# Kernel tuning notes

Hardware: AMD Instinct MI355X
Metric: run time of the kernel (lower is better)

## Reference

```python
import jax, jax.numpy as jnp
import numpy as np

T, H, I, E, TOPK = 4096, 2048, 4096, 8, 2


def setup_inputs() -> dict:
    key = jax.random.key(0)
    k0, k1, k2, k3, k4, k5 = jax.random.split(key, 6)
    return {
        "hidden_states": jax.random.normal(k0, (T, H), dtype=jnp.float32),
        "expert_affinities": jax.random.uniform(k1, (T, E), dtype=jnp.float32),
        "expert_index": jax.random.randint(k2, (T, TOPK), 0, E),
        "w_gate": jax.random.normal(k3, (E, H, I), dtype=jnp.float32) / np.float32(np.sqrt(H)),
        "w_up": jax.random.normal(k4, (E, H, I), dtype=jnp.float32) / np.float32(np.sqrt(H)),
        "w_down": jax.random.normal(k5, (E, I, H), dtype=jnp.float32) / np.float32(np.sqrt(I)),
    }


def reference(hidden_states, expert_affinities, expert_index, w_gate, w_up, w_down):
    num_experts = w_gate.shape[0]
    # top_k-hot mask (T, E); duplicate expert picks accumulate, matching torch loop
    expert_mask = jnp.sum(jax.nn.one_hot(expert_index, num_experts, dtype=jnp.float32), axis=1)
    # mask affinities to chosen experts, then L1-normalize (F.normalize p=1, eps=1e-12)
    aff = jnp.where(expert_mask == 0, 0.0, expert_affinities)
    aff = aff / jnp.maximum(jnp.sum(jnp.abs(aff), axis=1, keepdims=True), 1e-12)
    # all-experts GLU MLP: every expert processes all tokens
    g = jnp.einsum('th,ehi->eti', hidden_states, w_gate)   # (E, T, I)
    u = jnp.einsum('th,ehi->eti', hidden_states, w_up)     # (E, T, I)
    h = jax.nn.silu(g) * u                                  # (E, T, I)
    out_e = jnp.einsum('eti,eih->eth', h, w_down)           # (E, T, H)
    # affinity-weighted combine across experts
    return jnp.einsum('eth,te->th', out_e, aff)             # (T, H)
```

## Files before the change

### kernel.cpp

```cpp
#include <hip/hip_runtime.h>
#include <hip/hip_bf16.h>


constexpr int kT   = 4096;
constexpr int kH   = 2048;
constexpr int kI   = 4096;
constexpr int kE   = 8;
constexpr int kCap = 4096;
constexpr int kRowsCap = 10240;

typedef __attribute__((ext_vector_type(8))) short bf16x8;
typedef __attribute__((ext_vector_type(4))) float f32x4;

constexpr size_t HSB_OFF  = 0;
constexpr size_t HBUF_OFF = 16777216;
constexpr size_t RA_OFF   = HBUF_OFF + (size_t)kRowsCap * kI * 2;
constexpr size_t RB_OFF   = RA_OFF + (size_t)kE * kH * kI * 2;
constexpr size_t CNT_OFF  = RB_OFF + (size_t)kE * kH * kI * 2;
constexpr size_t OFF_OFF  = CNT_OFF + 256;
constexpr size_t LTOK_OFF = OFF_OFF + 256;
constexpr size_t LW_OFF   = LTOK_OFF + (size_t)kE * kCap * 4;
constexpr size_t POS_OFF  = LW_OFF + (size_t)kE * kCap * 4;
constexpr size_t WROW_OFF = POS_OFF + (size_t)kT * 2 * 4;

__device__ __forceinline__ unsigned short f2bf(float x) {
  unsigned int u = __float_as_uint(x);
  u += 0x7FFFu + ((u >> 16) & 1u);
  return (unsigned short)(u >> 16);
}
__device__ __forceinline__ unsigned pk2(float a, float b) {
  return (unsigned)f2bf(a) | ((unsigned)f2bf(b) << 16);
}
__device__ __forceinline__ float silu_f(float x) { return x / (1.f + __expf(-x)); }

__device__ __forceinline__ void async_copy16(void* lds, const void* g) {
  __builtin_amdgcn_global_load_lds(
      (const __attribute__((address_space(1))) void*)g,
      (__attribute__((address_space(3))) void*)lds, 16, 0, 0);
}

#define MFMA_BF16 __builtin_amdgcn_mfma_f32_16x16x32_bf16

__global__ void cvt_hs_kernel(const float* __restrict__ in, unsigned short* __restrict__ out) {
  size_t i = ((size_t)blockIdx.x * 256 + threadIdx.x) * 8;
  float4 a = *(const float4*)(in + i);
  float4 b = *(const float4*)(in + i + 4);
  uint4 v;
  v.x = pk2(a.x, a.y); v.y = pk2(a.z, a.w);
  v.z = pk2(b.x, b.y); v.w = pk2(b.z, b.w);
  *(uint4*)(out + i) = v;
}

__global__ __launch_bounds__(256)
void tcvt_kernel(const float* __restrict__ src, unsigned short* __restrict__ dst,
                 int K, int N) {
  __shared__ __attribute__((aligned(16))) unsigned short s[64][72];
  const size_t mat = (size_t)K * N;
  const float* S = src + (size_t)blockIdx.z * mat;
  unsigned short* D = dst + (size_t)blockIdx.z * mat;
  const int k0 = blockIdx.y * 64, n0 = blockIdx.x * 64;
  const int t  = threadIdx.x;
  const int n4 = (t & 15) * 4;
  const int k4 = (t >> 4) * 4;
  const float* p0 = S + (size_t)(k0 + k4) * N + n0 + n4;
  float4 r0 = *(const float4*)(p0);
  float4 r1 = *(const float4*)(p0 + N);
  float4 r2 = *(const float4*)(p0 + 2 * (size_t)N);
  float4 r3 = *(const float4*)(p0 + 3 * (size_t)N);
  uint2 v;
  v.x = pk2(r0.x, r1.x); v.y = pk2(r2.x, r3.x); *(uint2*)(&s[n4 + 0][k4]) = v;
  v.x = pk2(r0.y, r1.y); v.y = pk2(r2.y, r3.y); *(uint2*)(&s[n4 + 1][k4]) = v;
  v.x = pk2(r0.z, r1.z); v.y = pk2(r2.z, r3.z); *(uint2*)(&s[n4 + 2][k4]) = v;
  v.x = pk2(r0.w, r1.w); v.y = pk2(r2.w, r3.w); *(uint2*)(&s[n4 + 3][k4]) = v;
  __syncthreads();
  const int nn = t >> 3;
  const int kc = (t & 7) * 8;
#pragma unroll
  for (int i = 0; i < 2; ++i) {
    const int n = nn + i * 32;
    uint4 u = *(const uint4*)(&s[n][kc]);
    *(uint4*)(D + (size_t)(n0 + n) * K + k0 + kc) = u;
  }
}

__global__ void route_kernel(const float* __restrict__ aff, const int* __restrict__ idx,
                             int* counts, int* ltok, float* lw, int* pos) {
  int t = blockIdx.x * 256 + threadIdx.x;
  if (t >= kT) return;
  int e0 = idx[t * 2 + 0];
  int e1 = idx[t * 2 + 1];
  float a0 = aff[t * kE + e0];
  float a1 = aff[t * kE + e1];
  if (e0 == e1) {
    float w = a0 / fmaxf(fabsf(a0), 1e-12f);
    int s = atomicAdd(&counts[e0], 1);
    ltok[e0 * kCap + s] = t;
    lw[e0 * kCap + s]   = w;
    pos[t * 2 + 0] = (e0 << 12) | s;
    pos[t * 2 + 1] = -1;
  } else {
    float d = fmaxf(fabsf(a0) + fabsf(a1), 1e-12f);
    int s0 = atomicAdd(&counts[e0], 1);
    ltok[e0 * kCap + s0] = t;
    lw[e0 * kCap + s0]   = a0 / d;
    int s1 = atomicAdd(&counts[e1], 1);
    ltok[e1 * kCap + s1] = t;
    lw[e1 * kCap + s1]   = a1 / d;
    pos[t * 2 + 0] = (e0 << 12) | s0;
    pos[t * 2 + 1] = (e1 << 12) | s1;
  }
}

__global__ void prefix_kernel(const int* __restrict__ counts, int* offs) {
  if (threadIdx.x == 0 && blockIdx.x == 0) {
    int acc = 0;
    for (int e = 0; e < kE; ++e) { offs[e] = acc; acc += (counts[e] + 255) & ~255; }
  }
}

__global__ void wrow_kernel(const int* __restrict__ counts, const int* __restrict__ offs,
                            const float* __restrict__ lw, float* __restrict__ wrow) {
  int idx = blockIdx.x * 256 + threadIdx.x;
  int e = idx >> 12, s = idx & 4095;
  int cnt = counts[e];
  int al  = (cnt + 255) & ~255;
  if (s < al) wrow[offs[e] + s] = (s < cnt) ? lw[e * kCap + s] : 0.f;
}

__global__ __launch_bounds__(512, 2)
void gemm_gu_kernel(const unsigned short* __restrict__ hsb,
                    const unsigned short* __restrict__ wgT,
                    const unsigned short* __restrict__ wuT,
                    const int* __restrict__ counts, const int* __restrict__ offs,
                    const int* __restrict__ ltok, const float* __restrict__ wrow,
                    unsigned short* __restrict__ hbuf) {
  constexpr int NT = kH / 64;
  __shared__ __attribute__((aligned(16))) unsigned short lds[2 * 32768];

  const int e   = blockIdx.z;
  const int cnt = counts[e];
  const int m0  = blockIdx.y * 256;
  if (m0 >= cnt) return;
  const int n0   = blockIdx.x * 128;
  const int tid  = threadIdx.x;
  const int lane = tid & 63;
  const int wv   = tid >> 6;
  const int wm   = wv >> 2;
  const int wn   = wv & 3;
  const int baseRow = offs[e] + m0;

  const int skof = ((tid & 7) ^ ((tid >> 3) & 7)) * 8;
  const int r_   = tid >> 3;
  int s0 = m0 + r_;        s0 = s0 < cnt ? s0 : cnt - 1;
  int s1 = m0 + 64 + r_;   s1 = s1 < cnt ? s1 : cnt - 1;
  int s2 = m0 + 128 + r_;  s2 = s2 < cnt ? s2 : cnt - 1;
  int s3 = m0 + 192 + r_;  s3 = s3 < cnt ? s3 : cnt - 1;
  const unsigned short* aP0 = hsb + (size_t)ltok[e * kCap + s0] * kH + skof;
  const unsigned short* aP1 = hsb + (size_t)ltok[e * kCap + s1] * kH + skof;
  const unsigned short* aP2 = hsb + (size_t)ltok[e * kCap + s2] * kH + skof;
  const unsigned short* aP3 = hsb + (size_t)ltok[e * kCap + s3] * kH + skof;
  const unsigned short* wgP0 = wgT + (size_t)e * kI * kH + (size_t)(n0 + r_) * kH + skof;
  const unsigned short* wgP1 = wgT + (size_t)e * kI * kH + (size_t)(n0 + 64 + r_) * kH + skof;
  const unsigned short* wuP0 = wuT + (size_t)e * kI * kH + (size_t)(n0 + r_) * kH + skof;
  const unsigned short* wuP1 = wuT + (size_t)e * kI * kH + (size_t)(n0 + 64 + r_) * kH + skof;

  char* ldsb = (char*)lds;
  const int stO0 = tid * 16;
  const int stO1 = tid * 16 + 8192;
  const int ar  = lane & 15;
  const int lg  = lane >> 4;
  const int sk0 = ((lg ^ (lane & 7)) << 4);
  const int sk1 = (((4 + lg) ^ (lane & 7)) << 4);

  f32x4 accG[8][2] = {};
  f32x4 accU[8][2] = {};
  bf16x8 a0[4][2], a1[4][2], wgf[2][2], wuf[2][2];

#define STG2(dst, p0, p1, tt) {                                   \
    async_copy16((dst) + stO0, (p0) + (size_t)(tt) * 64);         \
    async_copy16((dst) + stO1, (p1) + (size_t)(tt) * 64); }
#define RD_A(dst, base, mh) _Pragma("unroll")                                  \
  for (int mf = 0; mf < 4; ++mf) {                                             \
    const char* rp_ = (base) + ((mh) * 128 + wm * 64 + mf * 16 + ar) * 128;    \
    dst[mf][0] = *(const bf16x8*)(rp_ + sk0);                                  \
    dst[mf][1] = *(const bf16x8*)(rp_ + sk1); }
#define RD_W(dst, base) _Pragma("unroll")                                      \
  for (int nf = 0; nf < 2; ++nf) {                                             \
    const char* rp_ = (base) + (wn * 32 + nf * 16 + ar) * 128;                 \
    dst[nf][0] = *(const bf16x8*)(rp_ + sk0);                                  \
    dst[nf][1] = *(const bf16x8*)(rp_ + sk1); }
#define MMA16(ACC, W, A, MH)                                                   \
  __builtin_amdgcn_s_setprio(1);                                               \
  _Pragma("unroll") for (int mf = 0; mf < 4; ++mf)                             \
    _Pragma("unroll") for (int nf = 0; nf < 2; ++nf) {                         \
      ACC[(MH)*4+mf][nf] = MFMA_BF16(W[nf][0], A[mf][0], ACC[(MH)*4+mf][nf], 0, 0, 0); \
      ACC[(MH)*4+mf][nf] = MFMA_BF16(W[nf][1], A[mf][1], ACC[(MH)*4+mf][nf], 0, 0, 0); \
    }                                                                          \
  __builtin_amdgcn_s_setprio(0);

#define GU_TILE(t, SA1, SM, VM)                                                \
  {                                                                            \
    char* bc = ldsb + ((t) & 1) * 65536;                                       \
    char* bo = ldsb + (((t) + 1) & 1) * 65536;                                 \
    RD_A(a0, bc, 0); RD_W(wgf, bc + 32768);                                    \
    if (SA1) STG2(bo + 16384, aP2, aP3, (t) + 1);                              \
    __builtin_amdgcn_s_barrier();                                              \
    MMA16(accG, wgf, a0, 0);                                                   \
    __builtin_amdgcn_s_barrier();                                              \
    RD_W(wuf, bc + 49152);                                                     \
    if (SM) STG2(bc, aP0, aP1, (t) + 2);                                       \
    __builtin_amdgcn_s_barrier();                                              \
    MMA16(accU, wuf, a0, 0);                                                   \
    __builtin_amdgcn_s_barrier();                                              \
    RD_A(a1, bc, 1);                                                           \
    if (SM) STG2(bc + 32768, wgP0, wgP1, (t) + 2);                             \
    __builtin_amdgcn_s_barrier();                                              \
    MMA16(accG, wgf, a1, 1);                                                   \
    __builtin_amdgcn_s_barrier();                                              \
    if (SM) STG2(bc + 49152, wuP0, wuP1, (t) + 2);                             \
    __builtin_amdgcn_s_barrier();                                              \
    MMA16(accU, wuf, a1, 1);                                                   \
    if ((VM) >= 0) {                                                           \
      asm volatile("s_waitcnt vmcnt(%0)" :: "i"((VM) < 0 ? 0 : (VM)) : "memory"); \
      __builtin_amdgcn_s_barrier();                                            \
    }                                                                          \
  }

  {
    char* b0 = ldsb;
    char* b1 = ldsb + 65536;
    STG2(b0,         aP0, aP1, 0);
    STG2(b0 + 16384, aP2, aP3, 0);
    STG2(b0 + 32768, wgP0, wgP1, 0);
    STG2(b0 + 49152, wuP0, wuP1, 0);
    STG2(b1,         aP0, aP1, 1);
    STG2(b1 + 32768, wgP0, wgP1, 1);
    STG2(b1 + 49152, wuP0, wuP1, 1);
    asm volatile("s_waitcnt vmcnt(6)" ::: "memory");
    __builtin_amdgcn_s_barrier();
  }

  for (int t = 0; t < NT - 2; ++t) GU_TILE(t, 1, 1, 6);
  GU_TILE(NT - 2, 1, 0, 0);
  GU_TILE(NT - 1, 0, 0, -1);
#undef GU_TILE

  const int lr4 = lg * 4;
#pragma unroll
  for (int mh = 0; mh < 2; ++mh)
#pragma unroll
    for (int mf = 0; mf < 4; ++mf) {
      const int grow = baseRow + mh * 128 + wm * 64 + mf * 16 + ar;
      const float wf = wrow[grow];
#pragma unroll
      for (int nf = 0; nf < 2; ++nf) {
        const int n = n0 + wn * 32 + nf * 16 + lr4;
        f32x4 g = accG[mh * 4 + mf][nf], u = accU[mh * 4 + mf][nf];
        float h0 = silu_f(g[0]) * u[0] * wf;
        float h1 = silu_f(g[1]) * u[1] * wf;
        float h2 = silu_f(g[2]) * u[2] * wf;
        float h3 = silu_f(g[3]) * u[3] * wf;
        uint2 v;
        v.x = pk2(h0, h1);
        v.y = pk2(h2, h3);
        *(uint2*)(hbuf + ((size_t)grow * kI + n)) = v;
      }
    }
#undef STG2
#undef RD_A
#undef RD_W
#undef MMA16
}

__global__ __launch_bounds__(512, 2)
void gemm_dn_kernel(const unsigned short* __restrict__ hbuf,
                    const unsigned short* __restrict__ wdT,
                    const int* __restrict__ counts, const int* __restrict__ offs,
                    float* __restrict__ obuf) {
  constexpr int NT = kI / 64;
  __shared__ __attribute__((aligned(16))) unsigned short lds[2 * 32768];

  const int e   = blockIdx.z;
  const int cnt = counts[e];
  const int m0  = blockIdx.y * 256;
  if (m0 >= cnt) return;
  const int n0   = blockIdx.x * 256;
  const int tid  = threadIdx.x;
  const int lane = tid & 63;
  const int wv   = tid >> 6;
  const int wm   = wv >> 2;
  const int wn   = wv & 3;
  const int baseRow = offs[e] + m0;

  const int skof = ((tid & 7) ^ ((tid >> 3) & 7)) * 8;
  const int r_   = tid >> 3;
  const unsigned short* aP0 = hbuf + (size_t)(baseRow + r_) * kI + skof;
  const unsigned short* aP1 = hbuf + (size_t)(baseRow + 64 + r_) * kI + skof;
  const unsigned short* aP2 = hbuf + (size_t)(baseRow + 128 + r_) * kI + skof;
  const unsigned short* aP3 = hbuf + (size_t)(baseRow + 192 + r_) * kI + skof;
  const unsigned short* wB = wdT + (size_t)e * kH * kI;
  const unsigned short* wP0 = wB + (size_t)(n0 + r_) * kI + skof;
  const unsigned short* wP1 = wB + (size_t)(n0 + 64 + r_) * kI + skof;
  const unsigned short* wP2 = wB + (size_t)(n0 + 128 + r_) * kI + skof;
  const unsigned short* wP3 = wB + (size_t)(n0 + 192 + r_) * kI + skof;

  char* ldsb = (char*)lds;
  const int stO0 = tid * 16;
  const int stO1 = tid * 16 + 8192;
  const int ar  = lane & 15;
  const int lg  = lane >> 4;
  const int sk0 = ((lg ^ (lane & 7)) << 4);
  const int sk1 = (((4 + lg) ^ (lane & 7)) << 4);

  f32x4 acc[8][4] = {};
  bf16x8 a0[4][2], a1[4][2], w0[2][2], w1[2][2];

#define STG2(dst, p0, p1, tt) {                                   \
    async_copy16((dst) + stO0, (p0) + (size_t)(tt) * 64);         \
    async_copy16((dst) + stO1, (p1) + (size_t)(tt) * 64); }
#define RD_A(dst, base, mh) _Pragma("unroll")                                  \
  for (int mf = 0; mf < 4; ++mf) {                                             \
    const char* rp_ = (base) + ((mh) * 128 + wm * 64 + mf * 16 + ar) * 128;    \
    dst[mf][0] = *(const bf16x8*)(rp_ + sk0);                                  \
    dst[mf][1] = *(const bf16x8*)(rp_ + sk1); }
#define RD_WN(dst, base, nh) _Pragma("unroll")                                 \
  for (int nf = 0; nf < 2; ++nf) {                                             \
    const char* rp_ = (base) + ((nh) * 128 + wn * 32 + nf * 16 + ar) * 128;    \
    dst[nf][0] = *(const bf16x8*)(rp_ + sk0);                                  \
    dst[nf][1] = *(const bf16x8*)(rp_ + sk1); }
#define MMA16(W, A, MH, NH)                                                    \
  __builtin_amdgcn_s_setprio(1);                                               \
  _Pragma("unroll") for (int mf = 0; mf < 4; ++mf)                             \
    _Pragma("unroll") for (int nf = 0; nf < 2; ++nf) {                         \
      acc[(MH)*4+mf][(NH)*2+nf] = MFMA_BF16(W[nf][0], A[mf][0], acc[(MH)*4+mf][(NH)*2+nf], 0, 0, 0); \
      acc[(MH)*4+mf][(NH)*2+nf] = MFMA_BF16(W[nf][1], A[mf][1], acc[(MH)*4+mf][(NH)*2+nf], 0, 0, 0); \
    }                                                                          \
  __builtin_amdgcn_s_setprio(0);

#define DN_TILE(t, SA1, SM, VM)                                                \
  {                                                                            \
    char* bc = ldsb + ((t) & 1) * 65536;                                       \
    char* bo = ldsb + (((t) + 1) & 1) * 65536;                                 \
    RD_A(a0, bc, 0); RD_WN(w0, bc + 32768, 0);                                 \
    if (SA1) STG2(bo + 16384, aP2, aP3, (t) + 1);                              \
    __builtin_amdgcn_s_barrier();                                              \
    MMA16(w0, a0, 0, 0);                                                       \
    __builtin_amdgcn_s_barrier();                                              \
    RD_WN(w1, bc + 32768, 1);                                                  \
    if (SM) STG2(bc, aP0, aP1, (t) + 2);                                       \
    __builtin_amdgcn_s_barrier();                                              \
    MMA16(w1, a0, 0, 1);                                                       \
    __builtin_amdgcn_s_barrier();                                              \
    RD_A(a1, bc, 1);                                                           \
    if (SM) STG2(bc + 32768, wP0, wP1, (t) + 2);                               \
    __builtin_amdgcn_s_barrier();                                              \
    MMA16(w0, a1, 1, 0);                                                       \
    __builtin_amdgcn_s_barrier();                                              \
    if (SM) STG2(bc + 49152, wP2, wP3, (t) + 2);                               \
    __builtin_amdgcn_s_barrier();                                              \
    MMA16(w1, a1, 1, 1);                                                       \
    if ((VM) >= 0) {                                                           \
      asm volatile("s_waitcnt vmcnt(%0)" :: "i"((VM) < 0 ? 0 : (VM)) : "memory"); \
      __builtin_amdgcn_s_barrier();                                            \
    }                                                                          \
  }

  {
    char* b0 = ldsb;
    char* b1 = ldsb + 65536;
    STG2(b0,         aP0, aP1, 0);
    STG2(b0 + 16384, aP2, aP3, 0);
    STG2(b0 + 32768, wP0, wP1, 0);
    STG2(b0 + 49152, wP2, wP3, 0);
    STG2(b1,         aP0, aP1, 1);
    STG2(b1 + 32768, wP0, wP1, 1);
    STG2(b1 + 49152, wP2, wP3, 1);
    asm volatile("s_waitcnt vmcnt(6)" ::: "memory");
    __builtin_amdgcn_s_barrier();
  }

  for (int t = 0; t < NT - 2; ++t) DN_TILE(t, 1, 1, 6);
  DN_TILE(NT - 2, 1, 0, 0);
  DN_TILE(NT - 1, 0, 0, -1);
#undef DN_TILE

  const int lr4 = lg * 4;
#pragma unroll
  for (int mh = 0; mh < 2; ++mh)
#pragma unroll
    for (int mf = 0; mf < 4; ++mf) {
      const int grow = baseRow + mh * 128 + wm * 64 + mf * 16 + ar;
#pragma unroll
      for (int nh = 0; nh < 2; ++nh)
#pragma unroll
        for (int nf = 0; nf < 2; ++nf) {
          const int n = n0 + nh * 128 + wn * 32 + nf * 16 + lr4;
          *(f32x4*)(obuf + (size_t)grow * kH + n) = acc[mh * 4 + mf][nh * 2 + nf];
        }
    }
#undef STG2
#undef RD_A
#undef RD_WN
#undef MMA16
}

__global__ void combine_kernel(const float* __restrict__ obuf,
                               const int* __restrict__ pos,
                               const int* __restrict__ offs,
                               float* __restrict__ out) {
  const int t   = blockIdx.y;
  const int col = blockIdx.x * 1024 + threadIdx.x * 4;
  const int c0  = pos[t * 2 + 0];
  const int c1  = pos[t * 2 + 1];
  const int row0 = offs[c0 >> 12] + (c0 & 4095);
  float4 v = *(const float4*)(obuf + (size_t)row0 * kH + col);
  if (c1 >= 0) {
    const int row1 = offs[c1 >> 12] + (c1 & 4095);
    float4 w = *(const float4*)(obuf + (size_t)row1 * kH + col);
    v.x += w.x; v.y += w.y; v.z += w.z; v.w += w.w;
  }
  *(float4*)(out + (size_t)t * kH + col) = v;
}

extern "C" void kernel_launch(void* const* d_in, const int* in_sizes, int n_in,
                              void* d_out, int out_size, void* d_ws, size_t ws_size,
                              hipStream_t stream) {
  const float* hs   = (const float*)d_in[0];
  const float* aff  = (const float*)d_in[1];
  const int*   eidx = (const int*)d_in[2];
  const float* wg   = (const float*)d_in[3];
  const float* wu   = (const float*)d_in[4];
  const float* wd   = (const float*)d_in[5];
  float* out = (float*)d_out;

  char* ws = (char*)d_ws;
  unsigned short* hsb  = (unsigned short*)(ws + HSB_OFF);
  unsigned short* hbuf = (unsigned short*)(ws + HBUF_OFF);
  unsigned short* wgT  = (unsigned short*)(ws + RA_OFF);
  unsigned short* wdT  = (unsigned short*)(ws + RA_OFF);
  unsigned short* wuT  = (unsigned short*)(ws + RB_OFF);
  float*          obuf = (float*)(ws + RB_OFF);
  int*            cnts = (int*)(ws + CNT_OFF);
  int*            offs = (int*)(ws + OFF_OFF);
  int*            ltok = (int*)(ws + LTOK_OFF);
  float*          lwgt = (float*)(ws + LW_OFF);
  int*            pos  = (int*)(ws + POS_OFF);
  float*          wrow = (float*)(ws + WROW_OFF);

  hipMemsetAsync(cnts, 0, kE * sizeof(int), stream);

  cvt_hs_kernel<<<(kT * kH) / (256 * 8), 256, 0, stream>>>(hs, hsb);
  route_kernel<<<kT / 256, 256, 0, stream>>>(aff, eidx, cnts, ltok, lwgt, pos);
  prefix_kernel<<<1, 64, 0, stream>>>(cnts, offs);
  wrow_kernel<<<(kE * kCap) / 256, 256, 0, stream>>>(cnts, offs, lwgt, wrow);

  tcvt_kernel<<<dim3(kI / 64, kH / 64, kE), 256, 0, stream>>>(wg, wgT, kH, kI);
  tcvt_kernel<<<dim3(kI / 64, kH / 64, kE), 256, 0, stream>>>(wu, wuT, kH, kI);

  gemm_gu_kernel<<<dim3(kI / 128, kCap / 256, kE), 512, 0, stream>>>(
      hsb, wgT, wuT, cnts, offs, ltok, wrow, hbuf);

  tcvt_kernel<<<dim3(kH / 64, kI / 64, kE), 256, 0, stream>>>(wd, wdT, kI, kH);

  gemm_dn_kernel<<<dim3(kH / 256, kCap / 256, kE), 512, 0, stream>>>(
      hbuf, wdT, cnts, offs, obuf);

  combine_kernel<<<dim3(kH / 1024, kT), 256, 0, stream>>>(obuf, pos, offs, out);
}
```

Baseline: 754.8 us.

## Fuse down-proj weight transpose into gate/up GEMM grid and shrink down-GEMM N tile

Result: faster. 718.2 us (-4.9%).

```diff
diff --git a/kernel.cpp b/kernel.cpp
--- a/kernel.cpp
+++ b/kernel.cpp
@@ -13,15 +13,18 @@
 typedef __attribute__((ext_vector_type(4))) float f32x4;
 
 constexpr size_t HSB_OFF  = 0;
-constexpr size_t HBUF_OFF = 16777216;
-constexpr size_t RA_OFF   = HBUF_OFF + (size_t)kRowsCap * kI * 2;
-constexpr size_t RB_OFF   = RA_OFF + (size_t)kE * kH * kI * 2;
-constexpr size_t CNT_OFF  = RB_OFF + (size_t)kE * kH * kI * 2;
-constexpr size_t OFF_OFF  = CNT_OFF + 256;
-constexpr size_t LTOK_OFF = OFF_OFF + 256;
+constexpr size_t CNT_OFF  = 16777216;
+constexpr size_t OFF_OFF  = CNT_OFF + 4096;
+constexpr size_t LTOK_OFF = OFF_OFF + 4096;
 constexpr size_t LW_OFF   = LTOK_OFF + (size_t)kE * kCap * 4;
 constexpr size_t POS_OFF  = LW_OFF + (size_t)kE * kCap * 4;
 constexpr size_t WROW_OFF = POS_OFF + (size_t)kT * 2 * 4;
+constexpr size_t HBUF_OFF = 17825792;
+constexpr size_t RA_OFF   = HBUF_OFF + (size_t)kRowsCap * kI * 2;
+constexpr size_t WMAT_B   = (size_t)kE * kH * kI * 2;
+constexpr size_t RB_OFF   = RA_OFF + WMAT_B;
+constexpr size_t WD_OFF   = RB_OFF + WMAT_B;
+constexpr size_t WS_NEED  = WD_OFF + WMAT_B;
 
 __device__ __forceinline__ unsigned short f2bf(float x) {
   unsigned int u = __float_as_uint(x);
@@ -127,15 +130,57 @@
   if (s < al) wrow[offs[e] + s] = (s < cnt) ? lw[e * kCap + s] : 0.f;
 }
 
+__device__ __forceinline__ void wd_path(const float* __restrict__ wd,
+                                        unsigned short* __restrict__ wdT,
+                                        int xp, int y, int z, int tid, char* ldsraw) {
+  const int q  = xp + 64 * y;
+  const int kt = q & 63, np = q >> 6;
+  const int K = kI, N = kH;
+  const float* S = wd + (size_t)z * K * N;
+  unsigned short* D = wdT + (size_t)z * K * N;
+  const int sub = tid >> 8, t = tid & 255;
+  const int k0 = kt * 64, n0 = np * 128 + sub * 64;
+  unsigned short (*s)[72] = (unsigned short(*)[72])(ldsraw + sub * 9216);
+  const int n4 = (t & 15) * 4;
+  const int k4 = (t >> 4) * 4;
+  const float* p0 = S + (size_t)(k0 + k4) * N + n0 + n4;
+  float4 r0 = *(const float4*)(p0);
+  float4 r1 = *(const float4*)(p0 + N);
+  float4 r2 = *(const float4*)(p0 + 2 * (size_t)N);
+  float4 r3 = *(const float4*)(p0 + 3 * (size_t)N);
+  uint2 v;
+  v.x = pk2(r0.x, r1.x); v.y = pk2(r2.x, r3.x); *(uint2*)(&s[n4 + 0][k4]) = v;
+  v.x = pk2(r0.y, r1.y); v.y = pk2(r2.y, r3.y); *(uint2*)(&s[n4 + 1][k4]) = v;
+  v.x = pk2(r0.z, r1.z); v.y = pk2(r2.z, r3.z); *(uint2*)(&s[n4 + 2][k4]) = v;
+  v.x = pk2(r0.w, r1.w); v.y = pk2(r2.w, r3.w); *(uint2*)(&s[n4 + 3][k4]) = v;
+  __syncthreads();
+  const int nn = t >> 3;
+  const int kc = (t & 7) * 8;
+#pragma unroll
+  for (int i = 0; i < 2; ++i) {
+    const int n = nn + i * 32;
+    uint4 u = *(const uint4*)(&s[n][kc]);
+    *(uint4*)(D + (size_t)(n0 + n) * K + k0 + kc) = u;
+  }
+}
+
 __global__ __launch_bounds__(512, 2)
 void gemm_gu_kernel(const unsigned short* __restrict__ hsb,
                     const unsigned short* __restrict__ wgT,
                     const unsigned short* __restrict__ wuT,
                     const int* __restrict__ counts, const int* __restrict__ offs,
                     const int* __restrict__ ltok, const float* __restrict__ wrow,
-                    unsigned short* __restrict__ hbuf) {
+                    unsigned short* __restrict__ hbuf,
+                    const float* __restrict__ wdSrc,
+                    unsigned short* __restrict__ wdDst) {
   constexpr int NT = kH / 64;
   __shared__ __attribute__((aligned(16))) unsigned short lds[2 * 32768];
+
+  if (blockIdx.x >= 32) {
+    wd_path(wdSrc, wdDst, blockIdx.x - 32, blockIdx.y, blockIdx.z,
+            threadIdx.x, (char*)lds);
+    return;
+  }
 
   const int e   = blockIdx.z;
   const int cnt = counts[e];
@@ -278,13 +323,13 @@
                     const int* __restrict__ counts, const int* __restrict__ offs,
                     float* __restrict__ obuf) {
   constexpr int NT = kI / 64;
-  __shared__ __attribute__((aligned(16))) unsigned short lds[2 * 32768];
+  __shared__ __attribute__((aligned(16))) unsigned short lds[2 * 24576];
 
   const int e   = blockIdx.z;
   const int cnt = counts[e];
   const int m0  = blockIdx.y * 256;
   if (m0 >= cnt) return;
-  const int n0   = blockIdx.x * 256;
+  const int n0   = blockIdx.x * 128;
   const int tid  = threadIdx.x;
   const int lane = tid & 63;
   const int wv   = tid >> 6;
@@ -301,8 +346,6 @@
   const unsigned short* wB = wdT + (size_t)e * kH * kI;
   const unsigned short* wP0 = wB + (size_t)(n0 + r_) * kI + skof;
   const unsigned short* wP1 = wB + (size_t)(n0 + 64 + r_) * kI + skof;
-  const unsigned short* wP2 = wB + (size_t)(n0 + 128 + r_) * kI + skof;
-  const unsigned short* wP3 = wB + (size_t)(n0 + 192 + r_) * kI + skof;
 
   char* ldsb = (char*)lds;
   const int stO0 = tid * 16;
@@ -312,8 +355,8 @@
   const int sk0 = ((lg ^ (lane & 7)) << 4);
   const int sk1 = (((4 + lg) ^ (lane & 7)) << 4);
 
-  f32x4 acc[8][4] = {};
-  bf16x8 a0[4][2], a1[4][2], w0[2][2], w1[2][2];
+  f32x4 acc[8][2] = {};
+  bf16x8 a0[4][2], a1[4][2], w0[2][2];
 
 #define STG2(dst, p0, p1, tt) {                                   \
     async_copy16((dst) + stO0, (p0) + (size_t)(tt) * 64);         \
@@ -323,42 +366,34 @@
     const char* rp_ = (base) + ((mh) * 128 + wm * 64 + mf * 16 + ar) * 128;    \
     dst[mf][0] = *(const bf16x8*)(rp_ + sk0);                                  \
     dst[mf][1] = *(const bf16x8*)(rp_ + sk1); }
-#define RD_WN(dst, base, nh) _Pragma("unroll")                                 \
+#define RD_W(dst, base) _Pragma("unroll")                                      \
   for (int nf = 0; nf < 2; ++nf) {                                             \
-    const char* rp_ = (base) + ((nh) * 128 + wn * 32 + nf * 16 + ar) * 128;    \
+    const char* rp_ = (base) + 32768 + (wn * 32 + nf * 16 + ar) * 128;         \
     dst[nf][0] = *(const bf16x8*)(rp_ + sk0);                                  \
     dst[nf][1] = *(const bf16x8*)(rp_ + sk1); }
-#define MMA16(W, A, MH, NH)                                                    \
+#define MMA16(A, MH)                                                           \
   __builtin_amdgcn_s_setprio(1);                                               \
   _Pragma("unroll") for (int mf = 0; mf < 4; ++mf)                             \
     _Pragma("unroll") for (int nf = 0; nf < 2; ++nf) {                         \
-      acc[(MH)*4+mf][(NH)*2+nf] = MFMA_BF16(W[nf][0], A[mf][0], acc[(MH)*4+mf][(NH)*2+nf], 0, 0, 0); \
-      acc[(MH)*4+mf][(NH)*2+nf] = MFMA_BF16(W[nf][1], A[mf][1], acc[(MH)*4+mf][(NH)*2+nf], 0, 0, 0); \
+      acc[(MH)*4+mf][nf] = MFMA_BF16(w0[nf][0], A[mf][0], acc[(MH)*4+mf][nf], 0, 0, 0); \
+      acc[(MH)*4+mf][nf] = MFMA_BF16(w0[nf][1], A[mf][1], acc[(MH)*4+mf][nf], 0, 0, 0); \
     }                                                                          \
   __builtin_amdgcn_s_setprio(0);
 
 #define DN_TILE(t, SA1, SM, VM)                                                \
   {                                                                            \
-    char* bc = ldsb + ((t) & 1) * 65536;                                       \
-    char* bo = ldsb + (((t) + 1) & 1) * 65536;                                 \
-    RD_A(a0, bc, 0); RD_WN(w0, bc + 32768, 0);                                 \
+    char* bc = ldsb + ((t) & 1) * 49152;                                       \
+    char* bo = ldsb + (((t) + 1) & 1) * 49152;                                 \
+    RD_A(a0, bc, 0); RD_W(w0, bc);                                             \
     if (SA1) STG2(bo + 16384, aP2, aP3, (t) + 1);                              \
     __builtin_amdgcn_s_barrier();                                              \
-    MMA16(w0, a0, 0, 0);                                                       \
-    __builtin_amdgcn_s_barrier();                                              \
-    RD_WN(w1, bc + 32768, 1);                                                  \
-    if (SM) STG2(bc, aP0, aP1, (t) + 2);                                       \
-    __builtin_amdgcn_s_barrier();                                              \
-    MMA16(w1, a0, 0, 1);                                                       \
+    MMA16(a0, 0);                                                              \
     __builtin_amdgcn_s_barrier();                                              \
     RD_A(a1, bc, 1);                                                           \
-    if (SM) STG2(bc + 32768, wP0, wP1, (t) + 2);                               \
-    __builtin_amdgcn_s_barrier();                                              \
-    MMA16(w0, a1, 1, 0);                                                       \
-    __builtin_amdgcn_s_barrier();                                              \
-    if (SM) STG2(bc + 49152, wP2, wP3, (t) + 2);                               \
-    __builtin_amdgcn_s_barrier();                                              \
-    MMA16(w1, a1, 1, 1);                                                       \
+    if (SM) { STG2(bc, aP0, aP1, (t) + 2);                                     \
+              STG2(bc + 32768, wP0, wP1, (t) + 2); }                           \
+    __builtin_amdgcn_s_barrier();                                              \
+    MMA16(a1, 1);                                                              \
     if ((VM) >= 0) {                                                           \
       asm volatile("s_waitcnt vmcnt(%0)" :: "i"((VM) < 0 ? 0 : (VM)) : "memory"); \
       __builtin_amdgcn_s_barrier();                                            \
@@ -367,19 +402,17 @@
 
   {
     char* b0 = ldsb;
-    char* b1 = ldsb + 65536;
+    char* b1 = ldsb + 49152;
     STG2(b0,         aP0, aP1, 0);
     STG2(b0 + 16384, aP2, aP3, 0);
     STG2(b0 + 32768, wP0, wP1, 0);
-    STG2(b0 + 49152, wP2, wP3, 0);
     STG2(b1,         aP0, aP1, 1);
     STG2(b1 + 32768, wP0, wP1, 1);
-    STG2(b1 + 49152, wP2, wP3, 1);
-    asm volatile("s_waitcnt vmcnt(6)" ::: "memory");
+    asm volatile("s_waitcnt vmcnt(4)" ::: "memory");
     __builtin_amdgcn_s_barrier();
   }
 
-  for (int t = 0; t < NT - 2; ++t) DN_TILE(t, 1, 1, 6);
+  for (int t = 0; t < NT - 2; ++t) DN_TILE(t, 1, 1, 4);
   DN_TILE(NT - 2, 1, 0, 0);
   DN_TILE(NT - 1, 0, 0, -1);
 #undef DN_TILE
@@ -391,16 +424,14 @@
     for (int mf = 0; mf < 4; ++mf) {
       const int grow = baseRow + mh * 128 + wm * 64 + mf * 16 + ar;
 #pragma unroll
-      for (int nh = 0; nh < 2; ++nh)
-#pragma unroll
-        for (int nf = 0; nf < 2; ++nf) {
-          const int n = n0 + nh * 128 + wn * 32 + nf * 16 + lr4;
-          *(f32x4*)(obuf + (size_t)grow * kH + n) = acc[mh * 4 + mf][nh * 2 + nf];
-        }
+      for (int nf = 0; nf < 2; ++nf) {
+        const int n = n0 + wn * 32 + nf * 16 + lr4;
+        *(f32x4*)(obuf + (size_t)grow * kH + n) = acc[mh * 4 + mf][nf];
+      }
     }
 #undef STG2
 #undef RD_A
-#undef RD_WN
+#undef RD_W
 #undef MMA16
 }
 
@@ -437,9 +468,7 @@
   unsigned short* hsb  = (unsigned short*)(ws + HSB_OFF);
   unsigned short* hbuf = (unsigned short*)(ws + HBUF_OFF);
   unsigned short* wgT  = (unsigned short*)(ws + RA_OFF);
-  unsigned short* wdT  = (unsigned short*)(ws + RA_OFF);
   unsigned short* wuT  = (unsigned short*)(ws + RB_OFF);
-  float*          obuf = (float*)(ws + RB_OFF);
   int*            cnts = (int*)(ws + CNT_OFF);
   int*            offs = (int*)(ws + OFF_OFF);
   int*            ltok = (int*)(ws + LTOK_OFF);
@@ -447,6 +476,12 @@
   int*            pos  = (int*)(ws + POS_OFF);
   float*          wrow = (float*)(ws + WROW_OFF);
 
+  const bool fused = (ws_size >= WS_NEED);
+  unsigned short* wdT  = fused ? (unsigned short*)(ws + WD_OFF)
+                               : (unsigned short*)(ws + RA_OFF);
+  float*          obuf = fused ? (float*)(ws + RA_OFF)
+                               : (float*)(ws + RB_OFF);
+
   hipMemsetAsync(cnts, 0, kE * sizeof(int), stream);
 
   cvt_hs_kernel<<<(kT * kH) / (256 * 8), 256, 0, stream>>>(hs, hsb);
@@ -457,12 +492,16 @@
   tcvt_kernel<<<dim3(kI / 64, kH / 64, kE), 256, 0, stream>>>(wg, wgT, kH, kI);
   tcvt_kernel<<<dim3(kI / 64, kH / 64, kE), 256, 0, stream>>>(wu, wuT, kH, kI);
 
-  gemm_gu_kernel<<<dim3(kI / 128, kCap / 256, kE), 512, 0, stream>>>(
-      hsb, wgT, wuT, cnts, offs, ltok, wrow, hbuf);
-
-  tcvt_kernel<<<dim3(kH / 64, kI / 64, kE), 256, 0, stream>>>(wd, wdT, kI, kH);
-
-  gemm_dn_kernel<<<dim3(kH / 256, kCap / 256, kE), 512, 0, stream>>>(
+  if (fused) {
+    gemm_gu_kernel<<<dim3(96, kCap / 256, kE), 512, 0, stream>>>(
+        hsb, wgT, wuT, cnts, offs, ltok, wrow, hbuf, wd, wdT);
+  } else {
+    gemm_gu_kernel<<<dim3(32, kCap / 256, kE), 512, 0, stream>>>(
+        hsb, wgT, wuT, cnts, offs, ltok, wrow, hbuf, nullptr, nullptr);
+    tcvt_kernel<<<dim3(kH / 64, kI / 64, kE), 256, 0, stream>>>(wd, wdT, kI, kH);
+  }
+
+  gemm_dn_kernel<<<dim3(kH / 128, kCap / 256, kE), 512, 0, stream>>>(
       hbuf, wdT, cnts, offs, obuf);
 
   combine_kernel<<<dim3(kH / 1024, kT), 256, 0, stream>>>(obuf, pos, offs, out);
```
